# Performance work log

Measured on AMD Instinct MI355X. Metric: run time of the kernel, lower is better.

## Reference

```python
import jax, jax.numpy as jnp
import numpy as np

B, C, F, H = 512, 80, 768, 256
EPS = 1e-5
THR = 0.5
SCALE = 1.0 / np.sqrt(H)


def _ln(z, g, b):
    m = jnp.mean(z, axis=-1, keepdims=True)
    v = jnp.mean((z - m) ** 2, axis=-1, keepdims=True)
    return (z - m) * jax.lax.rsqrt(v + EPS) * g + b


def setup_inputs() -> dict:
    key = jax.random.key(0)
    ks = jax.random.split(key, 12)
    w = 0.05  # weight scale for numerical sanity
    return {
        "x": jax.random.normal(ks[0], (B, C, H), jnp.float32),
        "visual_features": jax.random.normal(ks[1], (B, F), jnp.float32),
        "labels": jax.random.randint(ks[2], (B, C), 0, 2, jnp.int32),
        # visual_proj: Linear(F,H) + LayerNorm(H)
        "Wp": jax.random.normal(ks[3], (F, H), jnp.float32) * w,
        "bp": jnp.zeros((H,), jnp.float32),
        "gp": jnp.ones((H,), jnp.float32),
        "bep": jnp.zeros((H,), jnp.float32),
        # per-class extractors: stacked Linear(H,H) + LayerNorm(H)
        "Wc": jax.random.normal(ks[4], (C, H, H), jnp.float32) * w,
        "bc": jnp.zeros((C, H), jnp.float32),
        "gc": jnp.ones((C, H), jnp.float32),
        "bec": jnp.zeros((C, H), jnp.float32),
        # attention projections
        "Wq": jax.random.normal(ks[5], (H, H), jnp.float32) * w,
        "bq": jnp.zeros((H,), jnp.float32),
        "Wk": jax.random.normal(ks[6], (H, H), jnp.float32) * w,
        "bk": jnp.zeros((H,), jnp.float32),
        "Wv": jax.random.normal(ks[7], (H, H), jnp.float32) * w,
        "bv": jnp.zeros((H,), jnp.float32),
        "Wo": jax.random.normal(ks[8], (H, H), jnp.float32) * w,
        "bo": jnp.zeros((H,), jnp.float32),
    }


def reference(x, visual_features, labels, Wp, bp, gp, bep, Wc, bc, gc, bec,
              Wq, bq, Wk, bk, Wv, bv, Wo, bo):
    # visual_proj: Linear + LN + ReLU  -> (B,H)
    vis = jax.nn.relu(_ln(visual_features @ Wp + bp, gp, bep))
    # per-class extractor ensemble fused into one batched GEMM -> (B,C,H)
    z = jnp.einsum('bh,chk->bck', vis, Wc) + bc
    class_feats = jax.nn.relu(_ln(z, gc, bec))
    x = x + class_feats
    q = x @ Wq + bq
    k = x @ Wk + bk
    v = x @ Wv + bv
    scores = jnp.einsum('bch,bdh->bcd', q, k) * SCALE  # (B,C,C)
    scores = scores * (scores > THR).astype(scores.dtype)  # hard similarity mask
    label_mask = labels.astype(scores.dtype)[:, None, :] * 0.8 + 0.2
    scores = scores * label_mask
    attn = jax.nn.softmax(scores, axis=-1)
    out = jnp.einsum('bcd,bdh->bch', attn, v)
    return out @ Wo + bo
```

## Files before the change

### kernel.cpp

```cpp
#include <hip/hip_runtime.h>
#include <hip/hip_bf16.h>
#include <math.h>

#define Bq 512
#define Cq 80
#define Fq 768
#define Hq 256

constexpr float EPS   = 1e-5f;
constexpr float THR   = 0.5f;
constexpr float SCALE = 0.0625f;

using f32x4 = __attribute__((ext_vector_type(4))) float;
using s16x8 = __attribute__((ext_vector_type(8))) short;
using s16x4 = __attribute__((ext_vector_type(4))) short;

#define MFMA16 __builtin_amdgcn_mfma_f32_16x16x32_bf16


__device__ __forceinline__ float waveReduceSum(float v) {
#pragma unroll
  for (int m = 32; m >= 1; m >>= 1) v += __shfl_xor(v, m);
  return v;
}

__device__ __forceinline__ float bfu(unsigned short v) {
  return __uint_as_float(((unsigned)v) << 16);
}

__device__ __forceinline__ unsigned short f2bf(float f) {
  __hip_bfloat16 h = __float2bfloat16(f);
  return *reinterpret_cast<unsigned short*>(&h);
}

__device__ __forceinline__ int packOff(int tile, int kk8, int g, int l15, int e) {
  return ((tile * 8 + kk8) * 4 + g) * 128 + l15 * 8 + e;
}

__global__ __launch_bounds__(256) void k_visproj(
    const float* __restrict__ vf, const float* __restrict__ Wp,
    const float* __restrict__ bp, const float* __restrict__ gp,
    const float* __restrict__ bep,
    unsigned short* __restrict__ visPh, unsigned short* __restrict__ visPl) {
  __shared__ float vfs[Fq];
  __shared__ float red[4];
  const int b = blockIdx.x, h = threadIdx.x;
  for (int i = h; i < Fq; i += 256) vfs[i] = vf[b * Fq + i];
  __syncthreads();

  float acc = bp[h];
  for (int f = 0; f < Fq; f++) acc = fmaf(vfs[f], Wp[f * Hq + h], acc);

  const int w = h >> 6, lane = h & 63;
  float s = waveReduceSum(acc);
  if (lane == 0) red[w] = s;
  __syncthreads();
  const float mean = (red[0] + red[1] + red[2] + red[3]) * (1.0f / Hq);
  __syncthreads();
  const float d = acc - mean;
  s = waveReduceSum(d * d);
  if (lane == 0) red[w] = s;
  __syncthreads();
  const float var = (red[0] + red[1] + red[2] + red[3]) * (1.0f / Hq);
  float y = d * rsqrtf(var + EPS) * gp[h] + bep[h];
  y = fmaxf(y, 0.0f);
  const unsigned short hb = f2bf(y);
  const int off = packOff(b >> 4, h >> 5, (h & 31) >> 3, b & 15, h & 7);
  visPh[off] = hb;
  visPl[off] = f2bf(y - bfu(hb));
}

__global__ __launch_bounds__(256) void k_matmulM(
    const float* __restrict__ Wq, const float* __restrict__ Wk,
    const float* __restrict__ bq, const float* __restrict__ bk,
    unsigned short* __restrict__ MTph, unsigned short* __restrict__ MTpl,
    float* __restrict__ w1, float* __restrict__ w2, float* __restrict__ cqk) {
  const int i = blockIdx.x, j = threadIdx.x;
  const int wv = j >> 6, lane = j & 63;
  __shared__ float rowq[Hq];
  __shared__ float redA[4], redB[4], redC[4];
  rowq[j] = Wq[i * Hq + j];
  __syncthreads();
  float acc = 0.f;
  const float* wkr = Wk + (size_t)j * Hq;
  for (int h = 0; h < Hq; h += 4) {
    const float4 a = *reinterpret_cast<const float4*>(&rowq[h]);
    const float4 bb = *reinterpret_cast<const float4*>(&wkr[h]);
    acc = fmaf(a.x, bb.x, fmaf(a.y, bb.y, fmaf(a.z, bb.z, fmaf(a.w, bb.w, acc))));
  }
  const unsigned short hb = f2bf(acc);
  const int off = packOff(j >> 4, i >> 5, (i & 31) >> 3, j & 15, i & 7);
  MTph[off] = hb;
  MTpl[off] = f2bf(acc - bfu(hb));

  float p1 = rowq[j] * bk[j];
  float p2 = Wk[(size_t)i * Hq + j] * bq[j];
  float p3 = bq[j] * bk[j];
  p1 = waveReduceSum(p1);
  p2 = waveReduceSum(p2);
  p3 = waveReduceSum(p3);
  if (lane == 0) { redA[wv] = p1; redB[wv] = p2; redC[wv] = p3; }
  __syncthreads();
  if (j == 0) {
    w1[i] = redA[0] + redA[1] + redA[2] + redA[3];
    w2[i] = redB[0] + redB[1] + redB[2] + redB[3];
    if (i == 0) *cqk = redC[0] + redC[1] + redC[2] + redC[3];
  }
}

__global__ void k_prep(const float* __restrict__ Wc, const float* __restrict__ Wv,
                       const float* __restrict__ Wo,
                       unsigned short* __restrict__ WcTph, unsigned short* __restrict__ WcTpl,
                       unsigned short* __restrict__ WvTp, unsigned short* __restrict__ WoTp) {
  const int NWc = Cq * 32 * 256;
  const int NTOT = NWc + 2 * 32 * 256;
  for (int idx = blockIdx.x * blockDim.x + threadIdx.x; idx < NTOT;
       idx += gridDim.x * blockDim.x) {
    if (idx < NWc) {
      const int c = idx >> 13, k8 = (idx >> 8) & 31, n = idx & 255;
      const float* src = Wc + (size_t)c * 65536 + (size_t)k8 * 8 * 256 + n;
      s16x8 hh, ll;
#pragma unroll
      for (int e = 0; e < 8; e++) {
        const float v = src[e * 256];
        const unsigned short hb = f2bf(v);
        hh[e] = (short)hb;
        ll[e] = (short)f2bf(v - bfu(hb));
      }
      const int off = c * 65536 + packOff(n >> 4, k8 >> 2, k8 & 3, n & 15, 0);
      *reinterpret_cast<s16x8*>(WcTph + off) = hh;
      *reinterpret_cast<s16x8*>(WcTpl + off) = ll;
    } else {
      const int r = idx - NWc;
      const int which = r >> 13;
      const int r2 = r & 8191;
      const int k8 = r2 >> 8, n = r2 & 255;
      const float* src = (which == 0 ? Wv : Wo) + (size_t)k8 * 8 * 256 + n;
      s16x8 hh;
#pragma unroll
      for (int e = 0; e < 8; e++) hh[e] = (short)f2bf(src[e * 256]);
      const int off = packOff(n >> 4, k8 >> 2, k8 & 3, n & 15, 0);
      *reinterpret_cast<s16x8*>((which == 0 ? WvTp : WoTp) + off) = hh;
    }
  }
}

__global__ __launch_bounds__(256) void k_gemm1f(
    const unsigned short* __restrict__ visPh, const unsigned short* __restrict__ visPl,
    const unsigned short* __restrict__ WcTph, const unsigned short* __restrict__ WcTpl,
    const float* __restrict__ x, const float* __restrict__ bc,
    const float* __restrict__ gc, const float* __restrict__ bec,
    const float* __restrict__ w1, const float* __restrict__ w2,
    unsigned short* __restrict__ Xgh, unsigned short* __restrict__ Xgl,
    float* __restrict__ u, float* __restrict__ vv) {
  const int blk = blockIdx.x;
  const int mapped = (blk & 7) * 160 + (blk >> 3);
  const int c = mapped >> 4;
  const int bx = mapped & 15;
  const int b0 = bx * 32;
  const int tid = threadIdx.x;
  const int wvi = tid >> 6, lane = tid & 63;
  const int l15 = lane & 15, l4 = lane >> 4;

  __shared__ __attribute__((aligned(16))) float Zs[32][268];
  unsigned short* const Sh = reinterpret_cast<unsigned short*>(&Zs[0][0]);
  unsigned short* const Sl = Sh + 32 * 264;

  f32x4 acc[2][4];
#pragma unroll
  for (int m = 0; m < 2; m++)
#pragma unroll
    for (int n = 0; n < 4; n++) acc[m][n] = (f32x4){0.f, 0.f, 0.f, 0.f};

  const unsigned short* Bh = WcTph + (size_t)c * 65536;
  const unsigned short* Bl = WcTpl + (size_t)c * 65536;

  for (int kk8 = 0; kk8 < 8; kk8++) {
    s16x8 ah[2], al[2], bh[4], bl[4];
#pragma unroll
    for (int m = 0; m < 2; m++) {
      const int off = packOff(bx * 2 + m, kk8, l4, l15, 0);
      ah[m] = *reinterpret_cast<const s16x8*>(visPh + off);
      al[m] = *reinterpret_cast<const s16x8*>(visPl + off);
    }
#pragma unroll
    for (int n = 0; n < 4; n++) {
      const int off = packOff(wvi * 4 + n, kk8, l4, l15, 0);
      bh[n] = *reinterpret_cast<const s16x8*>(Bh + off);
      bl[n] = *reinterpret_cast<const s16x8*>(Bl + off);
    }
#pragma unroll
    for (int m = 0; m < 2; m++)
#pragma unroll
      for (int n = 0; n < 4; n++) {
        acc[m][n] = MFMA16(ah[m], bh[n], acc[m][n], 0, 0, 0);
        acc[m][n] = MFMA16(ah[m], bl[n], acc[m][n], 0, 0, 0);
        acc[m][n] = MFMA16(al[m], bh[n], acc[m][n], 0, 0, 0);
      }
  }

#pragma unroll
  for (int m = 0; m < 2; m++)
#pragma unroll
    for (int n = 0; n < 4; n++) {
      const int col = wvi * 64 + n * 16 + l15;
      const float bcv = bc[c * Hq + col];
#pragma unroll
      for (int r = 0; r < 4; r++)
        Zs[m * 16 + l4 * 4 + r][col] = acc[m][n][r] + bcv;
    }
  __syncthreads();

  const int row = tid >> 3, sub = tid & 7;
  const int grow = b0 + row;
  const size_t xrow = ((size_t)grow * Cq + c) * Hq;
  float zz[32];
  float sum = 0.f, sumsq = 0.f;
#pragma unroll
  for (int kq = 0; kq < 8; kq++) {
    const float4 z = *reinterpret_cast<const float4*>(&Zs[row][sub * 4 + kq * 32]);
    zz[4 * kq + 0] = z.x; zz[4 * kq + 1] = z.y;
    zz[4 * kq + 2] = z.z; zz[4 * kq + 3] = z.w;
    sum += z.x + z.y + z.z + z.w;
    sumsq += z.x * z.x + z.y * z.y + z.z * z.z + z.w * z.w;
  }
#pragma unroll
  for (int msk = 4; msk >= 1; msk >>= 1) {
    sum += __shfl_xor(sum, msk);
    sumsq += __shfl_xor(sumsq, msk);
  }
  const float mean = sum * (1.0f / Hq);
  const float var = sumsq * (1.0f / Hq) - mean * mean;
  const float inv = rsqrtf(var + EPS);
  __syncthreads();

  float pu = 0.f, pv = 0.f;
#pragma unroll
  for (int kq = 0; kq < 8; kq++) {
    const int col = sub * 4 + kq * 32;
    const float4 xv = *reinterpret_cast<const float4*>(&x[xrow + col]);
    const float xr[4] = {xv.x, xv.y, xv.z, xv.w};
    s16x4 hh, ll;
#pragma unroll
    for (int e = 0; e < 4; e++) {
      float tt = (zz[4 * kq + e] - mean) * inv * gc[c * Hq + col + e] + bec[c * Hq + col + e];
      tt = fmaxf(tt, 0.f);
      const float xp = xr[e] + tt;
      const unsigned short hb2 = f2bf(xp);
      hh[e] = (short)hb2;
      ll[e] = (short)f2bf(xp - bfu(hb2));
      pu = fmaf(xp, w1[col + e], pu);
      pv = fmaf(xp, w2[col + e], pv);
    }
    *reinterpret_cast<s16x4*>(&Sh[row * 264 + col]) = hh;
    *reinterpret_cast<s16x4*>(&Sl[row * 264 + col]) = ll;
  }
#pragma unroll
  for (int msk = 4; msk >= 1; msk >>= 1) {
    pu += __shfl_xor(pu, msk);
    pv += __shfl_xor(pv, msk);
  }
  if (sub == 0) {
    u[(size_t)grow * Cq + c] = pu;
    vv[(size_t)grow * Cq + c] = pv;
  }
  __syncthreads();

#pragma unroll
  for (int it = 0; it < 4; it++) {
    const int ch = it * 256 + tid;
    const int rr = ch >> 5, cc = ch & 31;
    const size_t gdst = ((size_t)(b0 + rr) * Cq + c) * Hq + cc * 8;
    *reinterpret_cast<s16x8*>(Xgh + gdst) = *reinterpret_cast<const s16x8*>(&Sh[rr * 264 + cc * 8]);
    *reinterpret_cast<s16x8*>(Xgl + gdst) = *reinterpret_cast<const s16x8*>(&Sl[rr * 264 + cc * 8]);
  }
}

__global__ __launch_bounds__(256) void k_gemm2p(
    unsigned short* Xh, unsigned short* Xl,
    const unsigned short* __restrict__ MTph, const unsigned short* __restrict__ MTpl,
    const unsigned short* __restrict__ WvTp, const float* __restrict__ bv,
    unsigned short* __restrict__ XMh, unsigned short* __restrict__ XMl,
    unsigned short* __restrict__ Vt) {
  __shared__ __attribute__((aligned(16))) unsigned short Xsh[32 * 264];
  __shared__ __attribute__((aligned(16))) unsigned short Xsl[32 * 264];
  __shared__ __attribute__((aligned(16))) unsigned short XMsh[8192];
  __shared__ __attribute__((aligned(16))) unsigned short XMsl[8192];
  __shared__ __attribute__((aligned(16))) unsigned short Vst[256 * 16];

  const int blk = blockIdx.x;
  const int r0 = blk * 32;
  const int tid = threadIdx.x;
  const int wvi = tid >> 6, lane = tid & 63;
  const int l15 = lane & 15, l4 = lane >> 4;

#pragma unroll
  for (int it = 0; it < 4; it++) {
    const int ch = it * 256 + tid;
    const int rr = ch >> 5, cc = ch & 31;
    const size_t gsrc = (size_t)(r0 + rr) * Hq + cc * 8;
    *reinterpret_cast<s16x8*>(&Xsh[rr * 264 + cc * 8]) =
        *reinterpret_cast<const s16x8*>(Xh + gsrc);
    *reinterpret_cast<s16x8*>(&Xsl[rr * 264 + cc * 8]) =
        *reinterpret_cast<const s16x8*>(Xl + gsrc);
  }
  __syncthreads();

  f32x4 acc[2][4];
#pragma unroll
  for (int m = 0; m < 2; m++)
#pragma unroll
    for (int n = 0; n < 4; n++) acc[m][n] = (f32x4){0.f, 0.f, 0.f, 0.f};

  for (int kk8 = 0; kk8 < 8; kk8++) {
    s16x8 ah[2], al[2], bh[4], bl[4];
#pragma unroll
    for (int m = 0; m < 2; m++) {
      const int lo = (m * 16 + l15) * 264 + kk8 * 32 + l4 * 8;
      ah[m] = *reinterpret_cast<const s16x8*>(&Xsh[lo]);
      al[m] = *reinterpret_cast<const s16x8*>(&Xsl[lo]);
    }
#pragma unroll
    for (int n = 0; n < 4; n++) {
      const int off = packOff(wvi * 4 + n, kk8, l4, l15, 0);
      bh[n] = *reinterpret_cast<const s16x8*>(MTph + off);
      bl[n] = *reinterpret_cast<const s16x8*>(MTpl + off);
    }
#pragma unroll
    for (int m = 0; m < 2; m++)
#pragma unroll
      for (int n = 0; n < 4; n++) {
        acc[m][n] = MFMA16(ah[m], bh[n], acc[m][n], 0, 0, 0);
        acc[m][n] = MFMA16(ah[m], bl[n], acc[m][n], 0, 0, 0);
        acc[m][n] = MFMA16(al[m], bh[n], acc[m][n], 0, 0, 0);
      }
  }

#pragma unroll
  for (int m = 0; m < 2; m++)
#pragma unroll
    for (int n = 0; n < 4; n++) {
      const int col = wvi * 64 + n * 16 + l15;
      const int kk8c = col >> 5, gc = (col & 31) >> 3, ec = col & 7;
#pragma unroll
      for (int r = 0; r < 4; r++) {
        const int off = ((m * 8 + kk8c) * 4 + gc) * 128 + (l4 * 4 + r) * 8 + ec;
        const float v = acc[m][n][r];
        const unsigned short hb = f2bf(v);
        XMsh[off] = hb;
        XMsl[off] = f2bf(v - bfu(hb));
      }
    }
  __syncthreads();

#pragma unroll
  for (int it = 0; it < 4; it++) {
    const int ch = it * 256 + tid;
    const size_t gdst = (size_t)blk * 8192 + ch * 8;
    *reinterpret_cast<s16x8*>(XMh + gdst) = *reinterpret_cast<const s16x8*>(&XMsh[ch * 8]);
    *reinterpret_cast<s16x8*>(XMl + gdst) = *reinterpret_cast<const s16x8*>(&XMsl[ch * 8]);
    const int l15c = ch & 15, g3 = (ch >> 4) & 3, kk = (ch >> 6) & 7, mm = ch >> 9;
    const int lsrc = (mm * 16 + l15c) * 264 + kk * 32 + g3 * 8;
    *reinterpret_cast<s16x8*>(Xh + gdst) = *reinterpret_cast<const s16x8*>(&Xsh[lsrc]);
    *reinterpret_cast<s16x8*>(Xl + gdst) = *reinterpret_cast<const s16x8*>(&Xsl[lsrc]);
  }

  for (int m = 0; m < 2; m++) {
    f32x4 vac[4];
#pragma unroll
    for (int n = 0; n < 4; n++) vac[n] = (f32x4){0.f, 0.f, 0.f, 0.f};
    for (int kk8 = 0; kk8 < 8; kk8++) {
      const int lo = (m * 16 + l15) * 264 + kk8 * 32 + l4 * 8;
      const s16x8 ah = *reinterpret_cast<const s16x8*>(&Xsh[lo]);
      const s16x8 al = *reinterpret_cast<const s16x8*>(&Xsl[lo]);
#pragma unroll
      for (int n = 0; n < 4; n++) {
        const s16x8 bh = *reinterpret_cast<const s16x8*>(
            WvTp + packOff(wvi * 4 + n, kk8, l4, l15, 0));
        vac[n] = MFMA16(ah, bh, vac[n], 0, 0, 0);
        vac[n] = MFMA16(al, bh, vac[n], 0, 0, 0);
      }
    }
#pragma unroll
    for (int n = 0; n < 4; n++) {
      const int col = (wvi * 4 + n) * 16 + l15;
      const float bvv = bv[col];
      s16x4 pk;
#pragma unroll
      for (int r = 0; r < 4; r++) pk[r] = (short)f2bf(vac[n][r] + bvv);
      *reinterpret_cast<s16x4*>(&Vst[col * 16 + l4 * 4]) = pk;
    }
    __syncthreads();
    {
      const int gt = blk * 2 + m;
#pragma unroll
      for (int it = 0; it < 2; it++) {
        const int ch = it * 256 + tid;
        *reinterpret_cast<s16x8*>(Vt + (size_t)gt * 4096 + ch * 8) =
            *reinterpret_cast<const s16x8*>(&Vst[ch * 8]);
      }
    }
    __syncthreads();
  }
}

__global__ __launch_bounds__(320) void k_attn6(
    const unsigned short* __restrict__ XPh, const unsigned short* __restrict__ XPl,
    const unsigned short* __restrict__ XMh, const unsigned short* __restrict__ XMl,
    const unsigned short* __restrict__ Vt, const int* __restrict__ labels,
    const float* __restrict__ u, const float* __restrict__ vv,
    const float* __restrict__ cqk, const unsigned short* __restrict__ WoTp,
    const float* __restrict__ bo, float* __restrict__ out) {
  __shared__ __attribute__((aligned(16))) unsigned short areaA[21120];
  __shared__ __attribute__((aligned(16))) unsigned short Pl_[80][104];
  __shared__ float us[80], vvs[80], lms[80];

  const int b = blockIdx.x, t = threadIdx.x;
  const int w = t >> 6, lane = t & 63;
  const int l15 = lane & 15, g = lane >> 4;
  const int tb = b * 5;

  if (t < 80) {
    us[t] = u[b * Cq + t];
    vvs[t] = vv[b * Cq + t];
    lms[t] = (float)labels[b * Cq + t] * 0.8f + 0.2f;
  }

  {
    s16x8 st[4];
#pragma unroll
    for (int q = 0; q < 4; q++) {
      const int j = 4 * w + q;
      const unsigned short* base = (j < 5) ? XPh : (j < 10) ? XPl : (j < 15) ? XMh : XMl;
      const int tile = tb + (j % 5);
      st[q] = *reinterpret_cast<const s16x8*>(base + (size_t)(tile * 8 + 0) * 512 + lane * 8);
    }
#pragma unroll
    for (int q = 0; q < 4; q++)
      *reinterpret_cast<s16x8*>(&areaA[(4 * w + q) * 512 + lane * 8]) = st[q];
  }
  __syncthreads();

  f32x4 sacc[5];
#pragma unroll
  for (int mt = 0; mt < 5; mt++) sacc[mt] = (f32x4){0.f, 0.f, 0.f, 0.f};

  int cur = 0;
  for (int kk8 = 0; kk8 < 8; kk8++) {
    s16x8 st[4];
    const bool pf = (kk8 < 7);
    if (pf) {
#pragma unroll
      for (int q = 0; q < 4; q++) {
        const int j = 4 * w + q;
        const unsigned short* base = (j < 5) ? XPh : (j < 10) ? XPl : (j < 15) ? XMh : XMl;
        const int tile = tb + (j % 5);
        st[q] = *reinterpret_cast<const s16x8*>(base + (size_t)(tile * 8 + kk8 + 1) * 512 + lane * 8);
      }
    }
    const unsigned short* B0 = &areaA[cur * 10240];
    const s16x8 bh = *reinterpret_cast<const s16x8*>(B0 + (10 + w) * 512 + lane * 8);
    const s16x8 bl = *reinterpret_cast<const s16x8*>(B0 + (15 + w) * 512 + lane * 8);
#pragma unroll
    for (int mt = 0; mt < 5; mt++) {
      const s16x8 ah = *reinterpret_cast<const s16x8*>(B0 + mt * 512 + lane * 8);
      const s16x8 al = *reinterpret_cast<const s16x8*>(B0 + (5 + mt) * 512 + lane * 8);
      sacc[mt] = MFMA16(ah, bh, sacc[mt], 0, 0, 0);
      sacc[mt] = MFMA16(ah, bl, sacc[mt], 0, 0, 0);
      sacc[mt] = MFMA16(al, bh, sacc[mt], 0, 0, 0);
    }
    if (pf) {
#pragma unroll
      for (int q = 0; q < 4; q++)
        *reinterpret_cast<s16x8*>(&areaA[(cur ^ 1) * 10240 + (4 * w + q) * 512 + lane * 8]) = st[q];
    }
    __syncthreads();
    cur ^= 1;
  }

  s16x8 vt[8];
  {
    const unsigned short* vsrc = Vt + (size_t)b * 20480;
#pragma unroll
    for (int q = 0; q < 8; q++)
      vt[q] = *reinterpret_cast<const s16x8*>(vsrc + (w * 8 + q) * 512 + lane * 8);
  }

  const int i = 16 * w + l15;
  const float ui = us[i];
  const float cq = *cqk;
  float p[5][4];
  float mx = -1e30f;
#pragma unroll
  for (int mt = 0; mt < 5; mt++)
#pragma unroll
    for (int r = 0; r < 4; r++) {
      const int j = 16 * mt + 4 * g + r;
      float sc = (sacc[mt][r] + ui + vvs[j] + cq) * SCALE;
      sc = (sc > THR) ? sc : 0.0f;
      sc *= lms[j];
      p[mt][r] = sc;
      mx = fmaxf(mx, sc);
    }
  mx = fmaxf(mx, __shfl_xor(mx, 16));
  mx = fmaxf(mx, __shfl_xor(mx, 32));
  float sum = 0.f;
#pragma unroll
  for (int mt = 0; mt < 5; mt++)
#pragma unroll
    for (int r = 0; r < 4; r++) {
      const float e = __expf(p[mt][r] - mx);
      p[mt][r] = e;
      sum += e;
    }
  sum += __shfl_xor(sum, 16);
  sum += __shfl_xor(sum, 32);
  const float inv = 1.0f / sum;

#pragma unroll
  for (int mt = 0; mt < 5; mt++) {
    uint2 pk;
    pk.x = (unsigned)f2bf(p[mt][0] * inv) | ((unsigned)f2bf(p[mt][1] * inv) << 16);
    pk.y = (unsigned)f2bf(p[mt][2] * inv) | ((unsigned)f2bf(p[mt][3] * inv) << 16);
    *reinterpret_cast<uint2*>(reinterpret_cast<char*>(&Pl_[i][0]) + 32 * mt + 8 * g) = pk;
  }
  if (t < 160) {
    const uint4 z = {0u, 0u, 0u, 0u};
    *reinterpret_cast<uint4*>(reinterpret_cast<char*>(&Pl_[t >> 1][0]) + 160 + 16 * (t & 1)) = z;
  }
#pragma unroll
  for (int q = 0; q < 8; q++)
    *reinterpret_cast<s16x8*>(&areaA[(w * 8 + q) * 512 + lane * 8]) = vt[q];
  __syncthreads();

  s16x8 pa[3];
#pragma unroll
  for (int ks = 0; ks < 3; ks++)
    pa[ks] = *reinterpret_cast<const s16x8*>(
        reinterpret_cast<const char*>(&Pl_[i][0]) + 64 * ks + 16 * g);

  f32x4 oacc[16];
#pragma unroll
  for (int n = 0; n < 16; n++) oacc[n] = (f32x4){0.f, 0.f, 0.f, 0.f};

#pragma unroll
  for (int n = 0; n < 16; n++) {
#pragma unroll
    for (int ks = 0; ks < 3; ks++) {
      const int c0 = 32 * ks + 8 * g;
      s16x8 vb = (s16x8){0, 0, 0, 0, 0, 0, 0, 0};
      if (c0 < 80) {
        const int ct = c0 >> 4, off = c0 & 15;
        vb = *reinterpret_cast<const s16x8*>(&areaA[ct * 4096 + (16 * n + l15) * 16 + off]);
      }
      oacc[n] = MFMA16(pa[ks], vb, oacc[n], 0, 0, 0);
    }
  }
  __syncthreads();

#pragma unroll
  for (int n = 0; n < 16; n++)
#pragma unroll
    for (int r = 0; r < 4; r++)
      areaA[(16 * w + 4 * g + r) * 264 + 16 * n + l15] = f2bf(oacc[n][r]);

  f32x4 acc2[16];
#pragma unroll
  for (int n = 0; n < 16; n++) acc2[n] = (f32x4){0.f, 0.f, 0.f, 0.f};

  for (int ks = 0; ks < 8; ks++) {
    const s16x8 af = *reinterpret_cast<const s16x8*>(
        &areaA[(16 * w + l15) * 264 + 32 * ks + 8 * g]);
    s16x8 bf[8];
#pragma unroll
    for (int n = 0; n < 8; n++)
      bf[n] = *reinterpret_cast<const s16x8*>(WoTp + packOff(n, ks, g, l15, 0));
#pragma unroll
    for (int n = 0; n < 8; n++) acc2[n] = MFMA16(af, bf[n], acc2[n], 0, 0, 0);
#pragma unroll
    for (int n = 0; n < 8; n++)
      bf[n] = *reinterpret_cast<const s16x8*>(WoTp + packOff(8 + n, ks, g, l15, 0));
#pragma unroll
    for (int n = 0; n < 8; n++) acc2[8 + n] = MFMA16(af, bf[n], acc2[8 + n], 0, 0, 0);
  }

  float* areaF = reinterpret_cast<float*>(areaA);
#pragma unroll
  for (int pp = 0; pp < 3; pp++) {
    const int cnt = (pp < 2) ? 32 : 16;
    __syncthreads();
    if ((w >> 1) == pp) {
      const int lr = 16 * w - 32 * pp;
#pragma unroll
      for (int n = 0; n < 16; n++) {
        const float bov = bo[16 * n + l15];
#pragma unroll
        for (int r = 0; r < 4; r++)
          areaF[(lr + 4 * g + r) * 264 + 16 * n + l15] = acc2[n][r] + bov;
      }
    }
    __syncthreads();
    for (int idx = t; idx < cnt * 64; idx += 320) {
      const int r = idx >> 6, c4 = (idx & 63) * 4;
      const float4 v4 = *reinterpret_cast<const float4*>(&areaF[r * 264 + c4]);
      *reinterpret_cast<float4*>(&out[((size_t)b * Cq + 32 * pp + r) * Hq + c4]) = v4;
    }
  }
}

extern "C" void kernel_launch(void* const* d_in, const int* in_sizes, int n_in,
                              void* d_out, int out_size, void* d_ws, size_t ws_size,
                              hipStream_t stream) {
  const float* x   = (const float*)d_in[0];
  const float* vf  = (const float*)d_in[1];
  const int*   lab = (const int*)d_in[2];
  const float* Wp  = (const float*)d_in[3];
  const float* bp  = (const float*)d_in[4];
  const float* gp  = (const float*)d_in[5];
  const float* bep = (const float*)d_in[6];
  const float* Wc  = (const float*)d_in[7];
  const float* bc  = (const float*)d_in[8];
  const float* gc  = (const float*)d_in[9];
  const float* bec = (const float*)d_in[10];
  const float* Wq  = (const float*)d_in[11];
  const float* bq_ = (const float*)d_in[12];
  const float* Wk  = (const float*)d_in[13];
  const float* bk_ = (const float*)d_in[14];
  const float* Wv  = (const float*)d_in[15];
  const float* bv_ = (const float*)d_in[16];
  const float* Wo  = (const float*)d_in[17];
  const float* bo_ = (const float*)d_in[18];
  float* out = (float*)d_out;
  (void)ws_size; (void)in_sizes; (void)n_in; (void)out_size;

  char* W = (char*)d_ws;
  unsigned short* Xh    = (unsigned short*)(W + 0);
  unsigned short* Xl    = (unsigned short*)(W + 20971520);
  unsigned short* WcTph = (unsigned short*)(W + 41943040);
  unsigned short* WcTpl = (unsigned short*)(W + 52428800);
  unsigned short* XMh   = (unsigned short*)(W + 41943040);
  unsigned short* XMl   = (unsigned short*)(W + 62914560);
  unsigned short* Vt    = (unsigned short*)(W + 83886080);
  unsigned short* visPh = (unsigned short*)(W + 104857600);
  unsigned short* visPl = (unsigned short*)(W + 105119744);
  unsigned short* MTph  = (unsigned short*)(W + 105381888);
  unsigned short* MTpl  = (unsigned short*)(W + 105512960);
  unsigned short* WvTp  = (unsigned short*)(W + 105644032);
  unsigned short* WoTp  = (unsigned short*)(W + 105775104);
  float* w1  = (float*)(W + 105906176);
  float* w2  = (float*)(W + 105907200);
  float* cqk = (float*)(W + 105908224);
  float* u   = (float*)(W + 105908480);
  float* vvv = (float*)(W + 106072320);

  k_visproj<<<Bq, 256, 0, stream>>>(vf, Wp, bp, gp, bep, visPh, visPl);
  k_matmulM<<<Hq, 256, 0, stream>>>(Wq, Wk, bq_, bk_, MTph, MTpl, w1, w2, cqk);
  k_prep<<<1024, 256, 0, stream>>>(Wc, Wv, Wo, WcTph, WcTpl, WvTp, WoTp);
  k_gemm1f<<<1280, 256, 0, stream>>>(visPh, visPl, WcTph, WcTpl, x, bc, gc, bec,
                                     w1, w2, Xh, Xl, u, vvv);
  k_gemm2p<<<1280, 256, 0, stream>>>(Xh, Xl, MTph, MTpl, WvTp, bv_,
                                     XMh, XMl, Vt);
  k_attn6<<<Bq, 320, 0, stream>>>(Xh, Xl, XMh, XMl, Vt, lab, u, vvv, cqk,
                                  WoTp, bo_, out);
}
```

Baseline: 207.1 us.

## Merge setup kernels, shrink gemm2p LDS via pooling, deepen QK prefetch in attention

```diff
diff --git a/kernel.cpp b/kernel.cpp
--- a/kernel.cpp
+++ b/kernel.cpp
@@ -37,110 +37,105 @@
   return ((tile * 8 + kk8) * 4 + g) * 128 + l15 * 8 + e;
 }
 
-__global__ __launch_bounds__(256) void k_visproj(
+__global__ __launch_bounds__(256) void k_setup(
     const float* __restrict__ vf, const float* __restrict__ Wp,
     const float* __restrict__ bp, const float* __restrict__ gp,
     const float* __restrict__ bep,
-    unsigned short* __restrict__ visPh, unsigned short* __restrict__ visPl) {
-  __shared__ float vfs[Fq];
-  __shared__ float red[4];
-  const int b = blockIdx.x, h = threadIdx.x;
-  for (int i = h; i < Fq; i += 256) vfs[i] = vf[b * Fq + i];
-  __syncthreads();
-
-  float acc = bp[h];
-  for (int f = 0; f < Fq; f++) acc = fmaf(vfs[f], Wp[f * Hq + h], acc);
-
-  const int w = h >> 6, lane = h & 63;
-  float s = waveReduceSum(acc);
-  if (lane == 0) red[w] = s;
-  __syncthreads();
-  const float mean = (red[0] + red[1] + red[2] + red[3]) * (1.0f / Hq);
-  __syncthreads();
-  const float d = acc - mean;
-  s = waveReduceSum(d * d);
-  if (lane == 0) red[w] = s;
-  __syncthreads();
-  const float var = (red[0] + red[1] + red[2] + red[3]) * (1.0f / Hq);
-  float y = d * rsqrtf(var + EPS) * gp[h] + bep[h];
-  y = fmaxf(y, 0.0f);
-  const unsigned short hb = f2bf(y);
-  const int off = packOff(b >> 4, h >> 5, (h & 31) >> 3, b & 15, h & 7);
-  visPh[off] = hb;
-  visPl[off] = f2bf(y - bfu(hb));
-}
-
-__global__ __launch_bounds__(256) void k_matmulM(
+    unsigned short* __restrict__ visPh, unsigned short* __restrict__ visPl,
     const float* __restrict__ Wq, const float* __restrict__ Wk,
     const float* __restrict__ bq, const float* __restrict__ bk,
     unsigned short* __restrict__ MTph, unsigned short* __restrict__ MTpl,
-    float* __restrict__ w1, float* __restrict__ w2, float* __restrict__ cqk) {
-  const int i = blockIdx.x, j = threadIdx.x;
-  const int wv = j >> 6, lane = j & 63;
-  __shared__ float rowq[Hq];
-  __shared__ float redA[4], redB[4], redC[4];
-  rowq[j] = Wq[i * Hq + j];
-  __syncthreads();
-  float acc = 0.f;
-  const float* wkr = Wk + (size_t)j * Hq;
-  for (int h = 0; h < Hq; h += 4) {
-    const float4 a = *reinterpret_cast<const float4*>(&rowq[h]);
-    const float4 bb = *reinterpret_cast<const float4*>(&wkr[h]);
-    acc = fmaf(a.x, bb.x, fmaf(a.y, bb.y, fmaf(a.z, bb.z, fmaf(a.w, bb.w, acc))));
-  }
-  const unsigned short hb = f2bf(acc);
-  const int off = packOff(j >> 4, i >> 5, (i & 31) >> 3, j & 15, i & 7);
-  MTph[off] = hb;
-  MTpl[off] = f2bf(acc - bfu(hb));
-
-  float p1 = rowq[j] * bk[j];
-  float p2 = Wk[(size_t)i * Hq + j] * bq[j];
-  float p3 = bq[j] * bk[j];
-  p1 = waveReduceSum(p1);
-  p2 = waveReduceSum(p2);
-  p3 = waveReduceSum(p3);
-  if (lane == 0) { redA[wv] = p1; redB[wv] = p2; redC[wv] = p3; }
-  __syncthreads();
-  if (j == 0) {
-    w1[i] = redA[0] + redA[1] + redA[2] + redA[3];
-    w2[i] = redB[0] + redB[1] + redB[2] + redB[3];
-    if (i == 0) *cqk = redC[0] + redC[1] + redC[2] + redC[3];
-  }
-}
-
-__global__ void k_prep(const float* __restrict__ Wc, const float* __restrict__ Wv,
-                       const float* __restrict__ Wo,
-                       unsigned short* __restrict__ WcTph, unsigned short* __restrict__ WcTpl,
-                       unsigned short* __restrict__ WvTp, unsigned short* __restrict__ WoTp) {
-  const int NWc = Cq * 32 * 256;
-  const int NTOT = NWc + 2 * 32 * 256;
-  for (int idx = blockIdx.x * blockDim.x + threadIdx.x; idx < NTOT;
-       idx += gridDim.x * blockDim.x) {
-    if (idx < NWc) {
-      const int c = idx >> 13, k8 = (idx >> 8) & 31, n = idx & 255;
-      const float* src = Wc + (size_t)c * 65536 + (size_t)k8 * 8 * 256 + n;
-      s16x8 hh, ll;
-#pragma unroll
-      for (int e = 0; e < 8; e++) {
-        const float v = src[e * 256];
-        const unsigned short hb = f2bf(v);
-        hh[e] = (short)hb;
-        ll[e] = (short)f2bf(v - bfu(hb));
+    float* __restrict__ w1, float* __restrict__ w2, float* __restrict__ cqk,
+    const float* __restrict__ Wc, const float* __restrict__ Wv,
+    const float* __restrict__ Wo,
+    unsigned short* __restrict__ WcTph, unsigned short* __restrict__ WcTpl,
+    unsigned short* __restrict__ WvTp, unsigned short* __restrict__ WoTp) {
+  __shared__ float smA[Fq];
+  __shared__ float red[4], redB[4], redC[4];
+  const int blk = blockIdx.x;
+
+  if (blk < 512) {
+    const int b = blk, h = threadIdx.x;
+    for (int i = h; i < Fq; i += 256) smA[i] = vf[b * Fq + i];
+    __syncthreads();
+    float acc = bp[h];
+    for (int f = 0; f < Fq; f++) acc = fmaf(smA[f], Wp[f * Hq + h], acc);
+    const int w = h >> 6, lane = h & 63;
+    float s = waveReduceSum(acc);
+    if (lane == 0) red[w] = s;
+    __syncthreads();
+    const float mean = (red[0] + red[1] + red[2] + red[3]) * (1.0f / Hq);
+    __syncthreads();
+    const float d = acc - mean;
+    s = waveReduceSum(d * d);
+    if (lane == 0) red[w] = s;
+    __syncthreads();
+    const float var = (red[0] + red[1] + red[2] + red[3]) * (1.0f / Hq);
+    float y = d * rsqrtf(var + EPS) * gp[h] + bep[h];
+    y = fmaxf(y, 0.0f);
+    const unsigned short hb = f2bf(y);
+    const int off = packOff(b >> 4, h >> 5, (h & 31) >> 3, b & 15, h & 7);
+    visPh[off] = hb;
+    visPl[off] = f2bf(y - bfu(hb));
+  } else if (blk < 768) {
+    const int i = blk - 512, j = threadIdx.x;
+    const int wv = j >> 6, lane = j & 63;
+    smA[j] = Wq[i * Hq + j];
+    __syncthreads();
+    float acc = 0.f;
+    const float* wkr = Wk + (size_t)j * Hq;
+    for (int h = 0; h < Hq; h += 4) {
+      const float4 a = *reinterpret_cast<const float4*>(&smA[h]);
+      const float4 bb = *reinterpret_cast<const float4*>(&wkr[h]);
+      acc = fmaf(a.x, bb.x, fmaf(a.y, bb.y, fmaf(a.z, bb.z, fmaf(a.w, bb.w, acc))));
+    }
+    const unsigned short hb = f2bf(acc);
+    const int off = packOff(j >> 4, i >> 5, (i & 31) >> 3, j & 15, i & 7);
+    MTph[off] = hb;
+    MTpl[off] = f2bf(acc - bfu(hb));
+    float p1 = smA[j] * bk[j];
+    float p2 = Wk[(size_t)i * Hq + j] * bq[j];
+    float p3 = bq[j] * bk[j];
+    p1 = waveReduceSum(p1);
+    p2 = waveReduceSum(p2);
+    p3 = waveReduceSum(p3);
+    if (lane == 0) { red[wv] = p1; redB[wv] = p2; redC[wv] = p3; }
+    __syncthreads();
+    if (j == 0) {
+      w1[i] = red[0] + red[1] + red[2] + red[3];
+      w2[i] = redB[0] + redB[1] + redB[2] + redB[3];
+      if (i == 0) *cqk = redC[0] + redC[1] + redC[2] + redC[3];
+    }
+  } else {
+    const int NWc = Cq * 32 * 256;
+    const int NTOT = NWc + 2 * 32 * 256;
+    for (int idx = (blk - 768) * 256 + threadIdx.x; idx < NTOT; idx += 1024 * 256) {
+      if (idx < NWc) {
+        const int c = idx >> 13, k8 = (idx >> 8) & 31, n = idx & 255;
+        const float* src = Wc + (size_t)c * 65536 + (size_t)k8 * 8 * 256 + n;
+        s16x8 hh, ll;
+#pragma unroll
+        for (int e = 0; e < 8; e++) {
+          const float v = src[e * 256];
+          const unsigned short hb = f2bf(v);
+          hh[e] = (short)hb;
+          ll[e] = (short)f2bf(v - bfu(hb));
+        }
+        const int off = c * 65536 + packOff(n >> 4, k8 >> 2, k8 & 3, n & 15, 0);
+        *reinterpret_cast<s16x8*>(WcTph + off) = hh;
+        *reinterpret_cast<s16x8*>(WcTpl + off) = ll;
+      } else {
+        const int r = idx - NWc;
+        const int which = r >> 13;
+        const int r2 = r & 8191;
+        const int k8 = r2 >> 8, n = r2 & 255;
+        const float* src = (which == 0 ? Wv : Wo) + (size_t)k8 * 8 * 256 + n;
+        s16x8 hh;
+#pragma unroll
+        for (int e = 0; e < 8; e++) hh[e] = (short)f2bf(src[e * 256]);
+        const int off = packOff(n >> 4, k8 >> 2, k8 & 3, n & 15, 0);
+        *reinterpret_cast<s16x8*>((which == 0 ? WvTp : WoTp) + off) = hh;
       }
-      const int off = c * 65536 + packOff(n >> 4, k8 >> 2, k8 & 3, n & 15, 0);
-      *reinterpret_cast<s16x8*>(WcTph + off) = hh;
-      *reinterpret_cast<s16x8*>(WcTpl + off) = ll;
-    } else {
-      const int r = idx - NWc;
-      const int which = r >> 13;
-      const int r2 = r & 8191;
-      const int k8 = r2 >> 8, n = r2 & 255;
-      const float* src = (which == 0 ? Wv : Wo) + (size_t)k8 * 8 * 256 + n;
-      s16x8 hh;
-#pragma unroll
-      for (int e = 0; e < 8; e++) hh[e] = (short)f2bf(src[e * 256]);
-      const int off = packOff(n >> 4, k8 >> 2, k8 & 3, n & 15, 0);
-      *reinterpret_cast<s16x8*>((which == 0 ? WvTp : WoTp) + off) = hh;
     }
   }
 }
@@ -276,23 +271,22 @@
   }
 }
 
-__global__ __launch_bounds__(256) void k_gemm2p(
+__global__ __launch_bounds__(256, 4) void k_gemm2p(
     unsigned short* Xh, unsigned short* Xl,
     const unsigned short* __restrict__ MTph, const unsigned short* __restrict__ MTpl,
     const unsigned short* __restrict__ WvTp, const float* __restrict__ bv,
     unsigned short* __restrict__ XMh, unsigned short* __restrict__ XMl,
     unsigned short* __restrict__ Vt) {
-  __shared__ __attribute__((aligned(16))) unsigned short Xsh[32 * 264];
-  __shared__ __attribute__((aligned(16))) unsigned short Xsl[32 * 264];
-  __shared__ __attribute__((aligned(16))) unsigned short XMsh[8192];
-  __shared__ __attribute__((aligned(16))) unsigned short XMsl[8192];
-  __shared__ __attribute__((aligned(16))) unsigned short Vst[256 * 16];
+  __shared__ __attribute__((aligned(16))) unsigned short pool[16896];
 
   const int blk = blockIdx.x;
   const int r0 = blk * 32;
   const int tid = threadIdx.x;
   const int wvi = tid >> 6, lane = tid & 63;
   const int l15 = lane & 15, l4 = lane >> 4;
+
+  unsigned short* const Xsh = pool;
+  unsigned short* const Xsl = pool + 8448;
 
 #pragma unroll
   for (int it = 0; it < 4; it++) {
@@ -336,6 +330,42 @@
       }
   }
 
+  f32x4 vac[2][4];
+#pragma unroll
+  for (int m = 0; m < 2; m++)
+#pragma unroll
+    for (int n = 0; n < 4; n++) vac[m][n] = (f32x4){0.f, 0.f, 0.f, 0.f};
+  for (int kk8 = 0; kk8 < 8; kk8++) {
+    s16x8 bhv[4];
+#pragma unroll
+    for (int n = 0; n < 4; n++)
+      bhv[n] = *reinterpret_cast<const s16x8*>(WvTp + packOff(wvi * 4 + n, kk8, l4, l15, 0));
+#pragma unroll
+    for (int m = 0; m < 2; m++) {
+      const int lo = (m * 16 + l15) * 264 + kk8 * 32 + l4 * 8;
+      const s16x8 ah = *reinterpret_cast<const s16x8*>(&Xsh[lo]);
+      const s16x8 al = *reinterpret_cast<const s16x8*>(&Xsl[lo]);
+#pragma unroll
+      for (int n = 0; n < 4; n++) {
+        vac[m][n] = MFMA16(ah, bhv[n], vac[m][n], 0, 0, 0);
+        vac[m][n] = MFMA16(al, bhv[n], vac[m][n], 0, 0, 0);
+      }
+    }
+  }
+
+#pragma unroll
+  for (int it = 0; it < 4; it++) {
+    const int ch = it * 256 + tid;
+    const size_t gdst = (size_t)blk * 8192 + ch * 8;
+    const int l15c = ch & 15, g3 = (ch >> 4) & 3, kk = (ch >> 6) & 7, mm = ch >> 9;
+    const int lsrc = (mm * 16 + l15c) * 264 + kk * 32 + g3 * 8;
+    *reinterpret_cast<s16x8*>(Xh + gdst) = *reinterpret_cast<const s16x8*>(&Xsh[lsrc]);
+    *reinterpret_cast<s16x8*>(Xl + gdst) = *reinterpret_cast<const s16x8*>(&Xsl[lsrc]);
+  }
+  __syncthreads();
+
+  unsigned short* const XMsh = pool;
+  unsigned short* const XMsl = pool + 8192;
 #pragma unroll
   for (int m = 0; m < 2; m++)
 #pragma unroll
@@ -359,52 +389,31 @@
     const size_t gdst = (size_t)blk * 8192 + ch * 8;
     *reinterpret_cast<s16x8*>(XMh + gdst) = *reinterpret_cast<const s16x8*>(&XMsh[ch * 8]);
     *reinterpret_cast<s16x8*>(XMl + gdst) = *reinterpret_cast<const s16x8*>(&XMsl[ch * 8]);
-    const int l15c = ch & 15, g3 = (ch >> 4) & 3, kk = (ch >> 6) & 7, mm = ch >> 9;
-    const int lsrc = (mm * 16 + l15c) * 264 + kk * 32 + g3 * 8;
-    *reinterpret_cast<s16x8*>(Xh + gdst) = *reinterpret_cast<const s16x8*>(&Xsh[lsrc]);
-    *reinterpret_cast<s16x8*>(Xl + gdst) = *reinterpret_cast<const s16x8*>(&Xsl[lsrc]);
-  }
-
-  for (int m = 0; m < 2; m++) {
-    f32x4 vac[4];
-#pragma unroll
-    for (int n = 0; n < 4; n++) vac[n] = (f32x4){0.f, 0.f, 0.f, 0.f};
-    for (int kk8 = 0; kk8 < 8; kk8++) {
-      const int lo = (m * 16 + l15) * 264 + kk8 * 32 + l4 * 8;
-      const s16x8 ah = *reinterpret_cast<const s16x8*>(&Xsh[lo]);
-      const s16x8 al = *reinterpret_cast<const s16x8*>(&Xsl[lo]);
-#pragma unroll
-      for (int n = 0; n < 4; n++) {
-        const s16x8 bh = *reinterpret_cast<const s16x8*>(
-            WvTp + packOff(wvi * 4 + n, kk8, l4, l15, 0));
-        vac[n] = MFMA16(ah, bh, vac[n], 0, 0, 0);
-        vac[n] = MFMA16(al, bh, vac[n], 0, 0, 0);
-      }
-    }
+  }
+  __syncthreads();
+
+  unsigned short* const Vst = pool;
+#pragma unroll
+  for (int m = 0; m < 2; m++)
 #pragma unroll
     for (int n = 0; n < 4; n++) {
       const int col = (wvi * 4 + n) * 16 + l15;
       const float bvv = bv[col];
       s16x4 pk;
 #pragma unroll
-      for (int r = 0; r < 4; r++) pk[r] = (short)f2bf(vac[n][r] + bvv);
-      *reinterpret_cast<s16x4*>(&Vst[col * 16 + l4 * 4]) = pk;
-    }
-    __syncthreads();
-    {
-      const int gt = blk * 2 + m;
-#pragma unroll
-      for (int it = 0; it < 2; it++) {
-        const int ch = it * 256 + tid;
-        *reinterpret_cast<s16x8*>(Vt + (size_t)gt * 4096 + ch * 8) =
-            *reinterpret_cast<const s16x8*>(&Vst[ch * 8]);
-      }
-    }
-    __syncthreads();
-  }
-}
-
-__global__ __launch_bounds__(320) void k_attn6(
+      for (int r = 0; r < 4; r++) pk[r] = (short)f2bf(vac[m][n][r] + bvv);
+      *reinterpret_cast<s16x4*>(&Vst[m * 4096 + col * 16 + l4 * 4]) = pk;
+    }
+  __syncthreads();
+#pragma unroll
+  for (int it = 0; it < 4; it++) {
+    const int ch = it * 256 + tid;
+    *reinterpret_cast<s16x8*>(Vt + (size_t)blk * 8192 + ch * 8) =
+        *reinterpret_cast<const s16x8*>(&Vst[ch * 8]);
+  }
+}
+
+__global__ __launch_bounds__(320) void k_attn7(
     const unsigned short* __restrict__ XPh, const unsigned short* __restrict__ XPl,
     const unsigned short* __restrict__ XMh, const unsigned short* __restrict__ XMl,
     const unsigned short* __restrict__ Vt, const int* __restrict__ labels,
@@ -426,57 +435,62 @@
     lms[t] = (float)labels[b * Cq + t] * 0.8f + 0.2f;
   }
 
-  {
-    s16x8 st[4];
-#pragma unroll
-    for (int q = 0; q < 4; q++) {
-      const int j = 4 * w + q;
-      const unsigned short* base = (j < 5) ? XPh : (j < 10) ? XPl : (j < 15) ? XMh : XMl;
-      const int tile = tb + (j % 5);
-      st[q] = *reinterpret_cast<const s16x8*>(base + (size_t)(tile * 8 + 0) * 512 + lane * 8);
-    }
-#pragma unroll
-    for (int q = 0; q < 4; q++)
-      *reinterpret_cast<s16x8*>(&areaA[(4 * w + q) * 512 + lane * 8]) = st[q];
-  }
-  __syncthreads();
+#define LOADSLICE(dst, KK)                                                      \
+  {                                                                             \
+    _Pragma("unroll")                                                           \
+    for (int q = 0; q < 4; q++) {                                               \
+      const int j = 4 * w + q;                                                  \
+      const unsigned short* base = (j < 5) ? XPh : (j < 10) ? XPl               \
+                                   : (j < 15) ? XMh : XMl;                      \
+      const int tile = tb + (j % 5);                                            \
+      dst[q] = *reinterpret_cast<const s16x8*>(                                 \
+          base + (size_t)(tile * 8 + (KK)) * 512 + lane * 8);                   \
+    }                                                                           \
+  }
+#define WRITESLICE(src, BUF)                                                    \
+  {                                                                             \
+    _Pragma("unroll")                                                           \
+    for (int q = 0; q < 4; q++)                                                 \
+      *reinterpret_cast<s16x8*>(                                                \
+          &areaA[(BUF) * 10240 + (4 * w + q) * 512 + lane * 8]) = src[q];       \
+  }
 
   f32x4 sacc[5];
 #pragma unroll
   for (int mt = 0; mt < 5; mt++) sacc[mt] = (f32x4){0.f, 0.f, 0.f, 0.f};
 
-  int cur = 0;
-  for (int kk8 = 0; kk8 < 8; kk8++) {
-    s16x8 st[4];
-    const bool pf = (kk8 < 7);
-    if (pf) {
-#pragma unroll
-      for (int q = 0; q < 4; q++) {
-        const int j = 4 * w + q;
-        const unsigned short* base = (j < 5) ? XPh : (j < 10) ? XPl : (j < 15) ? XMh : XMl;
-        const int tile = tb + (j % 5);
-        st[q] = *reinterpret_cast<const s16x8*>(base + (size_t)(tile * 8 + kk8 + 1) * 512 + lane * 8);
-      }
-    }
-    const unsigned short* B0 = &areaA[cur * 10240];
-    const s16x8 bh = *reinterpret_cast<const s16x8*>(B0 + (10 + w) * 512 + lane * 8);
-    const s16x8 bl = *reinterpret_cast<const s16x8*>(B0 + (15 + w) * 512 + lane * 8);
-#pragma unroll
-    for (int mt = 0; mt < 5; mt++) {
-      const s16x8 ah = *reinterpret_cast<const s16x8*>(B0 + mt * 512 + lane * 8);
-      const s16x8 al = *reinterpret_cast<const s16x8*>(B0 + (5 + mt) * 512 + lane * 8);
-      sacc[mt] = MFMA16(ah, bh, sacc[mt], 0, 0, 0);
-      sacc[mt] = MFMA16(ah, bl, sacc[mt], 0, 0, 0);
-      sacc[mt] = MFMA16(al, bh, sacc[mt], 0, 0, 0);
-    }
-    if (pf) {
-#pragma unroll
-      for (int q = 0; q < 4; q++)
-        *reinterpret_cast<s16x8*>(&areaA[(cur ^ 1) * 10240 + (4 * w + q) * 512 + lane * 8]) = st[q];
-    }
-    __syncthreads();
-    cur ^= 1;
-  }
+  s16x8 sA[4], sB[4];
+  LOADSLICE(sA, 0);
+  LOADSLICE(sB, 1);
+  WRITESLICE(sA, 0);
+  __syncthreads();
+
+#define QKSTEP(K, LD, WR)                                                       \
+  {                                                                             \
+    if ((K) < 6) LOADSLICE(LD, (K) + 2);                                        \
+    const unsigned short* B0 = &areaA[((K) & 1) * 10240];                       \
+    const s16x8 bh = *reinterpret_cast<const s16x8*>(B0 + (10 + w) * 512 + lane * 8);  \
+    const s16x8 bl = *reinterpret_cast<const s16x8*>(B0 + (15 + w) * 512 + lane * 8);  \
+    _Pragma("unroll")                                                           \
+    for (int mt = 0; mt < 5; mt++) {                                            \
+      const s16x8 ah = *reinterpret_cast<const s16x8*>(B0 + mt * 512 + lane * 8);      \
+      const s16x8 al = *reinterpret_cast<const s16x8*>(B0 + (5 + mt) * 512 + lane * 8);\
+      sacc[mt] = MFMA16(ah, bh, sacc[mt], 0, 0, 0);                             \
+      sacc[mt] = MFMA16(ah, bl, sacc[mt], 0, 0, 0);                             \
+      sacc[mt] = MFMA16(al, bh, sacc[mt], 0, 0, 0);                             \
+    }                                                                           \
+    if ((K) < 7) WRITESLICE(WR, ((K) + 1) & 1);                                 \
+    __syncthreads();                                                            \
+  }
+
+  QKSTEP(0, sA, sB)
+  QKSTEP(1, sB, sA)
+  QKSTEP(2, sA, sB)
+  QKSTEP(3, sB, sA)
+  QKSTEP(4, sA, sB)
+  QKSTEP(5, sB, sA)
+  QKSTEP(6, sA, sB)
+  QKSTEP(7, sB, sA)
 
   s16x8 vt[8];
   {
@@ -606,6 +620,9 @@
       *reinterpret_cast<float4*>(&out[((size_t)b * Cq + 32 * pp + r) * Hq + c4]) = v4;
     }
   }
+#undef QKSTEP
+#undef LOADSLICE
+#undef WRITESLICE
 }
 
 extern "C" void kernel_launch(void* const* d_in, const int* in_sizes, int n_in,
@@ -653,13 +670,13 @@
   float* u   = (float*)(W + 105908480);
   float* vvv = (float*)(W + 106072320);
 
-  k_visproj<<<Bq, 256, 0, stream>>>(vf, Wp, bp, gp, bep, visPh, visPl);
-  k_matmulM<<<Hq, 256, 0, stream>>>(Wq, Wk, bq_, bk_, MTph, MTpl, w1, w2, cqk);
-  k_prep<<<1024, 256, 0, stream>>>(Wc, Wv, Wo, WcTph, WcTpl, WvTp, WoTp);
+  k_setup<<<1792, 256, 0, stream>>>(vf, Wp, bp, gp, bep, visPh, visPl,
+                                    Wq, Wk, bq_, bk_, MTph, MTpl, w1, w2, cqk,
+                                    Wc, Wv, Wo, WcTph, WcTpl, WvTp, WoTp);
   k_gemm1f<<<1280, 256, 0, stream>>>(visPh, visPl, WcTph, WcTpl, x, bc, gc, bec,
                                      w1, w2, Xh, Xl, u, vvv);
   k_gemm2p<<<1280, 256, 0, stream>>>(Xh, Xl, MTph, MTpl, WvTp, bv_,
                                      XMh, XMl, Vt);
-  k_attn6<<<Bq, 320, 0, stream>>>(Xh, Xl, XMh, XMl, Vt, lab, u, vvv, cqk,
+  k_attn7<<<Bq, 320, 0, stream>>>(Xh, Xl, XMh, XMl, Vt, lab, u, vvv, cqk,
                                   WoTp, bo_, out);
 }
```

Result: slower. 241.9 us (+16.8%).
